# Kernel tuning notes

Measured on AMD Instinct MI355X. Metric: run time of the kernel, lower is better.

## Reference

```python
import jax, jax.numpy as jnp
import numpy as np

L, B, N = 2048, 128, 256
DT = 1.0 / L  # dt ~ 1/sequence_length per the docstring


def _hippo_legs(n):
    # transition('legs', n) from the original module
    q = np.arange(n, dtype=np.float64)
    col, row = np.meshgrid(q, q)
    r = 2 * q + 1
    M = -(np.where(row >= col, r, 0) - np.diag(q))
    T = np.sqrt(np.diag(2 * q + 1))
    A = T @ M @ np.linalg.inv(T)
    Bv = np.diag(T)  # (n,)
    return A, Bv


def _bilinear_discretize(A, Bv, dt):
    # scipy.signal.cont2discrete(..., method='bilinear')
    n = A.shape[0]
    I = np.eye(n)
    M = np.linalg.inv(I - (dt / 2.0) * A)
    dA = M @ (I + (dt / 2.0) * A)
    dB = (M @ (dt * Bv[:, None])).squeeze(-1)
    return dA, dB


def setup_inputs() -> dict:
    key = jax.random.key(0)
    A, Bv = _hippo_legs(N)
    dA, dB = _bilinear_discretize(A, Bv, DT)
    inputs = jax.random.normal(key, (L, B), dtype=jnp.float32)
    return {
        "inputs": inputs,
        "dA": jnp.asarray(dA, dtype=jnp.float32),
        "dB": jnp.asarray(dB, dtype=jnp.float32),
    }


def reference(inputs, dA, dB):
    # c_t = dA @ c_{t-1} + dB * f_t   (F.linear(c, dA) == c @ dA.T)
    n = dA.shape[0]
    c0 = jnp.zeros(inputs.shape[1:] + (n,), dtype=inputs.dtype)

    def step(c, f):
        c = c @ dA.T + f[..., None] * dB  # (B, N)
        return c, c

    _, cs = jax.lax.scan(step, c0, inputs)  # (L, B, N)
    return cs
```

## Files before the change

kernel.cpp:

```cpp
#include <hip/hip_runtime.h>
#include <hip/hip_cooperative_groups.h>
#include <stdint.h>
#include <stddef.h>

namespace cg = cooperative_groups;


typedef _Float16 f16;
typedef f16 half8 __attribute__((ext_vector_type(8)));
typedef float f32x4 __attribute__((ext_vector_type(4)));

#define SEQL 2048
#define NB 128
#define NS 256
#define PADROWS 64
#define LDA 72
#define LDB 72
#define LDC 280

#define SCAN0 56

__device__ __forceinline__ half8 h8zero() {
  half8 v;
#pragma unroll
  for (int u = 0; u < 8; u++) v[u] = (f16)0.f;
  return v;
}


__device__ __forceinline__ void stage_rows(f16* dst, int ld, int nrows,
                                           const f16* src, int sstride,
                                           int nvalid, int tid) {
  int tasks = nrows * 8;
  for (int i = tid; i < tasks; i += 512) {
    int row = i >> 3, c = (i & 7) << 3;
    half8 v = h8zero();
    if (row < nvalid) v = *(const half8*)(src + (size_t)row * sstride + c);
    *(half8*)(dst + row * ld + (c ^ (row & 56))) = v;
  }
}

__device__ __forceinline__ void stage_rows32(f16* dst, int ld, int nrows,
                                             const float* src, int sstride, int tid) {
  int tasks = nrows * 8;
  for (int i = tid; i < tasks; i += 512) {
    int row = i >> 3, c = (i & 7) << 3;
    const float* p = src + (size_t)row * sstride + c;
    half8 v;
#pragma unroll
    for (int u = 0; u < 8; u++) v[u] = (f16)p[u];
    *(half8*)(dst + row * ld + (c ^ (row & 56))) = v;
  }
}

__device__ __forceinline__ void stage_revtrans(f16* As, const f16* xpad,
                                               int s_top, int s_min, int tid) {
  for (int i = tid; i < 1024; i += 512) {
    int q = i >> 4, bb = (i & 15) << 3;
    int s = s_top - q;
    half8 v = h8zero();
    if (s >= s_min) v = *(const half8*)(xpad + (size_t)(PADROWS + s) * NB + bb);
#pragma unroll
    for (int u = 0; u < 8; u++) {
      int row = bb + u;
      As[row * LDA + (q ^ (row & 56))] = v[u];
    }
  }
}

__device__ __forceinline__ void stage_trans(f16* Bs, const f16* X, int c0, int tid) {
  for (int i = tid; i < 2048; i += 512) {
    int c = i >> 5, jj = (i & 31) << 3;
    half8 v = *(const half8*)(X + (size_t)(c0 + c) * NS + jj);
#pragma unroll
    for (int u = 0; u < 8; u++) {
      int row = jj + u;
      Bs[row * LDB + (c ^ (row & 56))] = v[u];
    }
  }
}

__device__ __forceinline__ void mm64(const f16* As, const f16* Bs,
                                     f32x4 acc[4][4], int wm, int wn,
                                     int l15, int quad) {
#pragma unroll
  for (int ks = 0; ks < 64; ks += 32) {
    half8 a[4], b[4];
#pragma unroll
    for (int ms = 0; ms < 4; ms++) {
      int ar = wm * 64 + ms * 16 + l15;
      a[ms] = *(const half8*)(As + ar * LDA + ((ks + quad * 8) ^ (ar & 56)));
    }
#pragma unroll
    for (int ns = 0; ns < 4; ns++) {
      int br = wn * 64 + ns * 16 + l15;
      b[ns] = *(const half8*)(Bs + br * LDB + ((ks + quad * 8) ^ (br & 56)));
    }
#pragma unroll
    for (int ms = 0; ms < 4; ms++)
#pragma unroll
      for (int ns = 0; ns < 4; ns++)
        acc[ms][ns] = __builtin_amdgcn_mfma_f32_16x16x32_f16(a[ms], b[ns], acc[ms][ns], 0, 0, 0);
  }
}

__device__ __forceinline__ void acc_zero(f32x4 acc[4][4]) {
#pragma unroll
  for (int ms = 0; ms < 4; ms++)
#pragma unroll
    for (int ns = 0; ns < 4; ns++)
#pragma unroll
      for (int u = 0; u < 4; u++) acc[ms][ns][u] = 0.f;
}

__device__ __forceinline__ void acc_store_split(const f32x4 acc[4][4], f16* H, f16* L,
                                                int rowoff, int wm, int wn, int l15, int quad) {
#pragma unroll
  for (int ms = 0; ms < 4; ms++)
#pragma unroll
    for (int ns = 0; ns < 4; ns++)
#pragma unroll
      for (int u = 0; u < 4; u++) {
        int row = rowoff + wm * 64 + ms * 16 + quad * 4 + u;
        int col = wn * 64 + ns * 16 + l15;
        float v = acc[ms][ns][u];
        f16 h = (f16)v;
        H[(size_t)row * NS + col] = h;
        L[(size_t)row * NS + col] = (f16)(v - (float)h);
      }
}

__device__ __forceinline__ void acc_store_f32(const f32x4 acc[4][4], float* dst,
                                              int wm, int wn, int l15, int quad) {
#pragma unroll
  for (int ms = 0; ms < 4; ms++)
#pragma unroll
    for (int ns = 0; ns < 4; ns++)
#pragma unroll
      for (int u = 0; u < 4; u++)
        dst[(size_t)(wm * 64 + ms * 16 + quad * 4 + u) * NS +
            wn * 64 + ns * 16 + l15] = acc[ms][ns][u];
}

__device__ __forceinline__ void product_split(const f16* AH, const f16* AL,
                                              const f16* BH, const f16* BL,
                                              f16* DH, f16* DL, int mtile,
                                              f16* As, f16* Bs,
                                              int tid, int wm, int wn, int l15, int quad) {
  f32x4 acc[4][4];
  acc_zero(acc);
#pragma unroll 1
  for (int pass = 0; pass < 3; pass++) {
    const f16* Asrc = (pass == 2) ? AL : AH;
    const f16* Bsrc = (pass == 1) ? BL : BH;
#pragma unroll 1
    for (int cc = 0; cc < 4; cc++) {
      stage_rows(As, LDA, 128, Asrc + (size_t)(mtile * 128) * NS + cc * 64, NS, 128, tid);
      stage_trans(Bs, Bsrc, cc * 64, tid);
      __syncthreads();
      mm64(As, Bs, acc, wm, wn, l15, quad);
      __syncthreads();
    }
  }
  acc_store_split(acc, DH, DL, mtile * 128, wm, wn, l15, quad);
}

__global__ void __launch_bounds__(512)
k_setup(const float* __restrict__ x, const float* __restrict__ dA,
        const float* __restrict__ dB,
        f16* __restrict__ PrH, f16* __restrict__ PrL,
        f16* __restrict__ Kt, f16* __restrict__ xpad,
        float* __restrict__ V0, float* __restrict__ V1) {
  cg::grid_group grid = cg::this_grid();
  __shared__ alignas(16) f16 As[128 * LDA];
  __shared__ alignas(16) f16 Bs[256 * LDB];
  __shared__ float dBs[NS];
  int tid = threadIdx.x;
  int lane = tid & 63, wid = tid >> 6;
  int wm = wid >> 2, wn = wid & 3;
  int l15 = lane & 15, quad = lane >> 4;
  int bi = blockIdx.x;

  {
    const int XPN = (PADROWS + SEQL) * NB;
    for (int g = bi * 512 + tid; g < XPN; g += 64 * 512) {
      int s = g >> 7;
      xpad[g] = (s < PADROWS) ? (f16)0.f : (f16)x[g - PADROWS * NB];
    }
    for (int g = bi * 512 + tid; g < NS * NS; g += 64 * 512) {
      float v = dA[g];
      f16 h = (f16)v;
      PrH[g] = h;
      PrL[g] = (f16)(v - (float)h);
    }
  }
  grid.sync();

#pragma unroll 1
  for (int m = 1; m <= 32; m <<= 1) {
    if (bi < 2 * m) {
      int prod = bi >> 1, mtile = bi & 1, r = prod + 1;
      product_split(PrH + (size_t)(m - 1) * 65536, PrL + (size_t)(m - 1) * 65536,
                    PrH + (size_t)(r - 1) * 65536, PrL + (size_t)(r - 1) * 65536,
                    PrH + (size_t)(m + r - 1) * 65536, PrL + (size_t)(m + r - 1) * 65536,
                    mtile, As, Bs, tid, wm, wn, l15, quad);
    }
    grid.sync();
  }

  {
    if (tid < NS) dBs[tid] = dB[tid];
    __syncthreads();
    int j = bi;
    if (tid < NS) {
      int n = tid;
      float a;
      if (j == 0) {
        a = dBs[n];
      } else {
        const f16* rh = PrH + (size_t)(j - 1) * 65536 + (size_t)n * NS;
        const f16* rl = PrL + (size_t)(j - 1) * 65536 + (size_t)n * NS;
        a = 0.f;
#pragma unroll 4
        for (int c = 0; c < NS; c += 8) {
          half8 vh = *(const half8*)(rh + c);
          half8 vl = *(const half8*)(rl + c);
#pragma unroll
          for (int u = 0; u < 8; u++) a += ((float)vh[u] + (float)vl[u]) * dBs[c + u];
        }
      }
      Kt[(size_t)n * 64 + j] = (f16)a;
    }
  }
  grid.sync();

  if (bi < 31) {
    int k = bi, t = 64 * k + 63;
    f32x4 acc[4][4];
    acc_zero(acc);
    stage_revtrans(As, xpad, t, 64 * k, tid);
    stage_rows(Bs, LDB, 256, Kt, 64, 256, tid);
    __syncthreads();
    mm64(As, Bs, acc, wm, wn, l15, quad);
    __syncthreads();
    acc_store_f32(acc, V0 + (size_t)k * 32768, wm, wn, l15, quad);
  }
  grid.sync();

  if (bi >= SCAN0) {
    int s = bi - SCAN0;
    int w = wid;
    const f16* SH = PrH + (size_t)63 * 65536;
    const f16* SL = PrL + (size_t)63 * 65536;
    half8 sfh[2][8], sfl[2][8];
#pragma unroll
    for (int nt = 0; nt < 2; nt++) {
      int n = (w * 2 + nt) * 16 + l15;
#pragma unroll
      for (int ks2 = 0; ks2 < 8; ks2++) {
        sfh[nt][ks2] = *(const half8*)(SH + (size_t)n * NS + ks2 * 32 + quad * 8);
        sfl[nt][ks2] = *(const half8*)(SL + (size_t)n * NS + ks2 * 32 + quad * 8);
      }
    }
    f16* Chi = As;
    f16* Clo = As + 16 * LDC;
    f32x4 acc2[2];
#pragma unroll 1
    for (int k = 0; k < 31; k++) {
#pragma unroll
      for (int nt = 0; nt < 2; nt++) {
        int col = (w * 2 + nt) * 16 + l15;
#pragma unroll
        for (int u = 0; u < 4; u++)
          acc2[nt][u] = V0[(size_t)k * 32768 + (size_t)(s * 16 + quad * 4 + u) * NS + col];
      }
      if (k > 0) {
#pragma unroll
        for (int ks2 = 0; ks2 < 8; ks2++) {
          half8 ah = *(const half8*)(Chi + l15 * LDC + ks2 * 32 + quad * 8);
          half8 al = *(const half8*)(Clo + l15 * LDC + ks2 * 32 + quad * 8);
#pragma unroll
          for (int nt = 0; nt < 2; nt++) {
            acc2[nt] = __builtin_amdgcn_mfma_f32_16x16x32_f16(ah, sfh[nt][ks2], acc2[nt], 0, 0, 0);
            acc2[nt] = __builtin_amdgcn_mfma_f32_16x16x32_f16(al, sfh[nt][ks2], acc2[nt], 0, 0, 0);
            acc2[nt] = __builtin_amdgcn_mfma_f32_16x16x32_f16(ah, sfl[nt][ks2], acc2[nt], 0, 0, 0);
          }
        }
      }
      __syncthreads();
#pragma unroll
      for (int nt = 0; nt < 2; nt++) {
        int col = (w * 2 + nt) * 16 + l15;
#pragma unroll
        for (int u = 0; u < 4; u++) {
          int row = quad * 4 + u;
          float v = acc2[nt][u];
          f16 h = (f16)v;
          Chi[row * LDC + col] = h;
          Clo[row * LDC + col] = (f16)(v - (float)h);
          V1[(size_t)k * 32768 + (size_t)(s * 16 + row) * NS + col] = v;
        }
      }
      __syncthreads();
    }
  }
}

__global__ void k_pass2(const f16* __restrict__ PrH, const f16* __restrict__ Kt,
                        const f16* __restrict__ xpad, const float* __restrict__ Vfin,
                        float* __restrict__ out) {
  __shared__ alignas(16) f16 As[128 * LDA];
  __shared__ alignas(16) f16 Bs[256 * LDB];
  int tid = threadIdx.x;
  int lane = tid & 63, wid = tid >> 6;
  int wm = wid >> 2, wn = wid & 3;
  int l15 = lane & 15, quad = lane >> 4;
  int bi = blockIdx.x;
  int r = bi >> 5, k = bi & 31;
  int t = 64 * k + r;
  const f16* G = PrH + (size_t)r * 65536;
  f32x4 acc[4][4];
  acc_zero(acc);
  if (k > 0) {
    const float* C = Vfin + (size_t)(k - 1) * 32768;
#pragma unroll 1
    for (int cc = 0; cc < 4; cc++) {
      stage_rows32(As, LDA, 128, C + cc * 64, NS, tid);
      stage_rows(Bs, LDB, 256, G + cc * 64, NS, 256, tid);
      __syncthreads();
      mm64(As, Bs, acc, wm, wn, l15, quad);
      __syncthreads();
    }
  }
  stage_revtrans(As, xpad, t, 64 * k, tid);
  stage_rows(Bs, LDB, 256, Kt, 64, 256, tid);
  __syncthreads();
  mm64(As, Bs, acc, wm, wn, l15, quad);
  __syncthreads();
  acc_store_f32(acc, out + (size_t)t * (NB * NS), wm, wn, l15, quad);
}

extern "C" void kernel_launch(void* const* d_in, const int* in_sizes, int n_in,
                              void* d_out, int out_size, void* d_ws, size_t ws_size,
                              hipStream_t stream) {
  const float* x = (const float*)d_in[0];
  const float* dA = (const float*)d_in[1];
  const float* dB = (const float*)d_in[2];
  float* out = (float*)d_out;

  char* ws = (char*)d_ws;
  f16* PrH = (f16*)(ws + 0);
  f16* PrL = (f16*)(ws + 8388608);
  f16* Kt  = (f16*)(ws + 17825792);
  f16* Xp  = (f16*)(ws + 17858560);
  float* V0 = (float*)(ws + 18399232);
  float* V1 = (float*)(ws + 22462464);

  void* args[] = {&x, &dA, &dB, &PrH, &PrL, &Kt, &Xp, &V0, &V1};
  hipLaunchCooperativeKernel(reinterpret_cast<void*>(k_setup), dim3(64), dim3(512),
                             args, 0, stream);
  k_pass2<<<2048, 512, 0, stream>>>(PrH, Kt, Xp, V1, out);
}
```

Measured before the change: 633.1 us.

## Register-prefetch next tiles during MFMA in product and pass2 GEMM loops

```diff
diff --git a/kernel.cpp b/kernel.cpp
--- a/kernel.cpp
+++ b/kernel.cpp
@@ -68,17 +68,53 @@
   }
 }
 
-__device__ __forceinline__ void stage_trans(f16* Bs, const f16* X, int c0, int tid) {
-  for (int i = tid; i < 2048; i += 512) {
-    int c = i >> 5, jj = (i & 31) << 3;
-    half8 v = *(const half8*)(X + (size_t)(c0 + c) * NS + jj);
-#pragma unroll
-    for (int u = 0; u < 8; u++) {
-      int row = jj + u;
-      Bs[row * LDB + (c ^ (row & 56))] = v[u];
-    }
-  }
-}
+
+template <int NT>
+struct RowsPrefetch {
+  half8 v[NT];
+  __device__ __forceinline__ void load(const f16* src, int sstride, int nvalid, int tid) {
+#pragma unroll
+    for (int j = 0; j < NT; j++) {
+      int i = tid + j * 512;
+      int row = i >> 3, c = (i & 7) << 3;
+      v[j] = (row < nvalid) ? *(const half8*)(src + (size_t)row * sstride + c)
+                            : h8zero();
+    }
+  }
+  __device__ __forceinline__ void store(f16* dst, int ld, int tid) {
+#pragma unroll
+    for (int j = 0; j < NT; j++) {
+      int i = tid + j * 512;
+      int row = i >> 3, c = (i & 7) << 3;
+      *(half8*)(dst + row * ld + (c ^ (row & 56))) = v[j];
+    }
+  }
+};
+
+template <int NT>
+struct TransPrefetch {
+  half8 v[NT];
+  __device__ __forceinline__ void load(const f16* X, int c0, int tid) {
+#pragma unroll
+    for (int j = 0; j < NT; j++) {
+      int i = tid + j * 512;
+      int c = i >> 5, jj = (i & 31) << 3;
+      v[j] = *(const half8*)(X + (size_t)(c0 + c) * NS + jj);
+    }
+  }
+  __device__ __forceinline__ void store(f16* Bs, int tid) {
+#pragma unroll
+    for (int j = 0; j < NT; j++) {
+      int i = tid + j * 512;
+      int c = i >> 5, jj = (i & 31) << 3;
+#pragma unroll
+      for (int u = 0; u < 8; u++) {
+        int row = jj + u;
+        Bs[row * LDB + (c ^ (row & 56))] = v[j][u];
+      }
+    }
+  }
+};
 
 __device__ __forceinline__ void mm64(const f16* As, const f16* Bs,
                                      f32x4 acc[4][4], int wm, int wn,
@@ -142,25 +178,45 @@
             wn * 64 + ns * 16 + l15] = acc[ms][ns][u];
 }
 
-__device__ __forceinline__ void product_split(const f16* AH, const f16* AL,
-                                              const f16* BH, const f16* BL,
-                                              f16* DH, f16* DL, int mtile,
-                                              f16* As, f16* Bs,
-                                              int tid, int wm, int wn, int l15, int quad) {
+__device__ __forceinline__ void product_split_pipe(const f16* AH, const f16* AL,
+                                                   const f16* BH, const f16* BL,
+                                                   f16* DH, f16* DL, int mtile,
+                                                   f16* As, f16* Bs,
+                                                   int tid, int wm, int wn,
+                                                   int l15, int quad) {
   f32x4 acc[4][4];
   acc_zero(acc);
+  RowsPrefetch<2> ap;
+  TransPrefetch<4> bp;
+  const size_t arow = (size_t)(mtile * 128) * NS;
+  ap.load(AL + arow, NS, 128, tid);
+  bp.load(BH, 0, tid);
+  ap.store(As, LDA, tid);
+  bp.store(Bs, tid);
+  __syncthreads();
 #pragma unroll 1
-  for (int pass = 0; pass < 3; pass++) {
-    const f16* Asrc = (pass == 2) ? AL : AH;
-    const f16* Bsrc = (pass == 1) ? BL : BH;
-#pragma unroll 1
-    for (int cc = 0; cc < 4; cc++) {
-      stage_rows(As, LDA, 128, Asrc + (size_t)(mtile * 128) * NS + cc * 64, NS, 128, tid);
-      stage_trans(Bs, Bsrc, cc * 64, tid);
-      __syncthreads();
-      mm64(As, Bs, acc, wm, wn, l15, quad);
-      __syncthreads();
-    }
+  for (int s = 0; s < 12; s++) {
+    int sn = s + 1;
+    int restA = 0, restB = 0;
+    if (sn < 12) {
+      int c3 = sn % 3, ccn = sn / 3;
+      if (c3 == 0) {
+        ap.load(AL + arow + ccn * 64, NS, 128, tid);
+        bp.load(BH, ccn * 64, tid);
+        restA = restB = 1;
+      } else if (c3 == 1) {
+        ap.load(AH + arow + ccn * 64, NS, 128, tid);
+        restA = 1;
+      } else {
+        bp.load(BL, ccn * 64, tid);
+        restB = 1;
+      }
+    }
+    mm64(As, Bs, acc, wm, wn, l15, quad);
+    __syncthreads();
+    if (restA) ap.store(As, LDA, tid);
+    if (restB) bp.store(Bs, tid);
+    __syncthreads();
   }
   acc_store_split(acc, DH, DL, mtile * 128, wm, wn, l15, quad);
 }
@@ -200,10 +256,10 @@
   for (int m = 1; m <= 32; m <<= 1) {
     if (bi < 2 * m) {
       int prod = bi >> 1, mtile = bi & 1, r = prod + 1;
-      product_split(PrH + (size_t)(m - 1) * 65536, PrL + (size_t)(m - 1) * 65536,
-                    PrH + (size_t)(r - 1) * 65536, PrL + (size_t)(r - 1) * 65536,
-                    PrH + (size_t)(m + r - 1) * 65536, PrL + (size_t)(m + r - 1) * 65536,
-                    mtile, As, Bs, tid, wm, wn, l15, quad);
+      product_split_pipe(PrH + (size_t)(m - 1) * 65536, PrL + (size_t)(m - 1) * 65536,
+                         PrH + (size_t)(r - 1) * 65536, PrL + (size_t)(r - 1) * 65536,
+                         PrH + (size_t)(m + r - 1) * 65536, PrL + (size_t)(m + r - 1) * 65536,
+                         mtile, As, Bs, tid, wm, wn, l15, quad);
     }
     grid.sync();
   }
@@ -306,9 +362,10 @@
   }
 }
 
-__global__ void k_pass2(const f16* __restrict__ PrH, const f16* __restrict__ Kt,
-                        const f16* __restrict__ xpad, const float* __restrict__ Vfin,
-                        float* __restrict__ out) {
+__global__ void __launch_bounds__(512, 4)
+k_pass2(const f16* __restrict__ PrH, const f16* __restrict__ Kt,
+        const f16* __restrict__ xpad, const float* __restrict__ Vfin,
+        float* __restrict__ out) {
   __shared__ alignas(16) f16 As[128 * LDA];
   __shared__ alignas(16) f16 Bs[256 * LDB];
   int tid = threadIdx.x;
@@ -323,20 +380,29 @@
   acc_zero(acc);
   if (k > 0) {
     const float* C = Vfin + (size_t)(k - 1) * 32768;
+    RowsPrefetch<4> bp;
+    bp.load(G, NS, 256, tid);
+    stage_rows32(As, LDA, 128, C, NS, tid);
+    bp.store(Bs, LDB, tid);
+    __syncthreads();
 #pragma unroll 1
     for (int cc = 0; cc < 4; cc++) {
-      stage_rows32(As, LDA, 128, C + cc * 64, NS, tid);
-      stage_rows(Bs, LDB, 256, G + cc * 64, NS, 256, tid);
-      __syncthreads();
+      if (cc < 3) bp.load(G + (cc + 1) * 64, NS, 256, tid);
+      else        bp.load(Kt, 64, 256, tid);
       mm64(As, Bs, acc, wm, wn, l15, quad);
       __syncthreads();
-    }
-  }
-  stage_revtrans(As, xpad, t, 64 * k, tid);
-  stage_rows(Bs, LDB, 256, Kt, 64, 256, tid);
-  __syncthreads();
-  mm64(As, Bs, acc, wm, wn, l15, quad);
-  __syncthreads();
+      bp.store(Bs, LDB, tid);
+      if (cc < 3) stage_rows32(As, LDA, 128, C + (cc + 1) * 64, NS, tid);
+      else        stage_revtrans(As, xpad, t, 64 * k, tid);
+      __syncthreads();
+    }
+    mm64(As, Bs, acc, wm, wn, l15, quad);
+  } else {
+    stage_revtrans(As, xpad, t, 64 * k, tid);
+    stage_rows(Bs, LDB, 256, Kt, 64, 256, tid);
+    __syncthreads();
+    mm64(As, Bs, acc, wm, wn, l15, quad);
+  }
   acc_store_f32(acc, out + (size_t)t * (NB * NS), wm, wn, l15, quad);
 }
 
```

Result: faster. 616.7 us (-2.6%).
